# Performance work log

Measured on AMD Instinct MI355X. Metric: run time of the kernel, lower is better.

## Reference

```python
import jax, jax.numpy as jnp
import numpy as np

B, N, F = 8, 512, 128
H, U = 4, 32
LEAKY_ALPHA = 0.2

def setup_inputs() -> dict:
    key = jax.random.key(0)
    k1, k2, k3, k4 = jax.random.split(key, 4)
    inputs = jax.random.normal(k1, (B, N, F), dtype=jnp.float32)
    # glorot-ish scaled params
    W_src = jax.random.normal(k2, (H, F, U), dtype=jnp.float32) * (2.0 / (F + U)) ** 0.5
    W_dst = jax.random.normal(k3, (H, F, U), dtype=jnp.float32) * (2.0 / (F + U)) ** 0.5
    a = jax.random.normal(k4, (H, U, 1), dtype=jnp.float32) * (2.0 / (U + 1)) ** 0.5
    return {"inputs": inputs, "W_src": W_src, "W_dst": W_dst, "a": a}

def reference(inputs, W_src, W_dst, a):
    # GATv2, eval mode (no dropout). Loop over the small fixed head count to
    # keep peak memory at one (B,N,N,U) pairwise tensor at a time, matching
    # the original per-head loop.
    outs = []
    for h in range(W_src.shape[0]):
        h_src = inputs @ W_src[h]          # (B, N, U)
        h_dst = inputs @ W_dst[h]          # (B, N, U)
        # pairwise[b,i,j,:] = h_src[b,i] + h_dst[b,j]
        pair = jax.nn.leaky_relu(h_src[:, :, None, :] + h_dst[:, None, :, :],
                                 negative_slope=LEAKY_ALPHA)  # (B,N,N,U)
        scores = jnp.einsum('biju,u->bij', pair, a[h, :, 0])   # (B,N,N)
        attn = jax.nn.softmax(scores, axis=-1)
        outs.append(attn @ h_src)          # (B,N,U) -- weighted sum of h_src
    return jnp.concatenate(outs, axis=-1)  # concat_heads=True -> (B,N,H*U)
```

## Files before the change

### kernel.cpp

```cpp
#include <hip/hip_runtime.h>
#include <hip/hip_bf16.h>

#define B_ 8
#define N_ 512
#define F_ 128
#define H_ 4
#define U_ 32
#define LEAKY_ALPHA 0.2f
#define PS 520

typedef __attribute__((ext_vector_type(8))) short short8;
typedef __attribute__((ext_vector_type(4))) float f32x4;

static __device__ __forceinline__ short f2bf_s(float x) {
    __hip_bfloat16 hv = __float2bfloat16(x);
    return *reinterpret_cast<short*>(&hv);
}
static __device__ __forceinline__ float bf2f_s(short v) {
    return __uint_as_float(((unsigned)(unsigned short)v) << 16);
}

__global__ __launch_bounds__(256) void proj_kernel(
    const float* __restrict__ x, const float* __restrict__ Wsrc,
    const float* __restrict__ Wdst, const float* __restrict__ a,
    float* __restrict__ hsrc, float* __restrict__ hdstNT,
    float* __restrict__ Drow, float* __restrict__ ascaled,
    short* __restrict__ hsrcT)
{
    __shared__ float4 xlds[8 * 32];
    const int t  = threadIdx.x;
    const int r0 = blockIdx.x * 8;

    const float4* xg = (const float4*)x + (size_t)r0 * 32;
    xlds[t] = xg[t];
    __syncthreads();

    const int u     = t & 31;
    const int h     = (t >> 5) & 3;
    const int which = t >> 7;
    const float* W  = (which ? Wdst : Wsrc) + h * (F_ * U_) + u;

    float acc[8];
#pragma unroll
    for (int r = 0; r < 8; ++r) acc[r] = 0.f;

#pragma unroll 2
    for (int fc = 0; fc < 32; ++fc) {
        const float w0 = W[(4 * fc + 0) * U_];
        const float w1 = W[(4 * fc + 1) * U_];
        const float w2 = W[(4 * fc + 2) * U_];
        const float w3 = W[(4 * fc + 3) * U_];
#pragma unroll
        for (int r = 0; r < 8; ++r) {
            const float4 xv = xlds[r * 32 + fc];
            float s = acc[r];
            s = fmaf(xv.x, w0, s);
            s = fmaf(xv.y, w1, s);
            s = fmaf(xv.z, w2, s);
            s = fmaf(xv.w, w3, s);
            acc[r] = s;
        }
    }

    const float av = a[h * U_ + u];
    if (which == 1 && blockIdx.x == 0)
        ascaled[h * U_ + u] = (1.f - LEAKY_ALPHA) * av;

    const int b  = r0 >> 9;
    const int n0 = r0 & (N_ - 1);
    const int bh = b * H_ + h;

    if (which == 0) {
        short8 pk;
#pragma unroll
        for (int r = 0; r < 8; ++r) {
            const size_t base = ((size_t)(bh * N_ + n0 + r) << 5) + u;
            hsrc[base] = acc[r];
            pk[r] = f2bf_s(acc[r]);
        }
        *(short8*)&hsrcT[((size_t)(bh * U_) + u) * N_ + n0] = pk;
    } else {
        float4 v0, v1;
        v0.x = -acc[0]; v0.y = -acc[1]; v0.z = -acc[2]; v0.w = -acc[3];
        v1.x = -acc[4]; v1.y = -acc[5]; v1.z = -acc[6]; v1.w = -acc[7];
        float* dst = hdstNT + ((size_t)(bh * U_) + u) * N_ + n0;
        *(float4*)dst       = v0;
        *(float4*)(dst + 4) = v1;
#pragma unroll
        for (int r = 0; r < 8; ++r) {
            float v = acc[r] * av;
            v += __shfl_xor(v, 1);
            v += __shfl_xor(v, 2);
            v += __shfl_xor(v, 4);
            v += __shfl_xor(v, 8);
            v += __shfl_xor(v, 16);
            if (u == 0) Drow[bh * N_ + n0 + r] = v;
        }
    }
}

__global__ __launch_bounds__(512, 4) void attn_kernel(
    const float* __restrict__ hsrc, const float* __restrict__ hdstNT,
    const float* __restrict__ Drow, const float* __restrict__ ascaled,
    const short* __restrict__ hsrcT, float* __restrict__ out)
{
    __shared__ __align__(16) short pbf[16 * PS];
    __shared__ f32x4 scr[8][64];
    __shared__ float lfin[16];

    const int t    = threadIdx.x;
    const int L    = t & 63;
    const int w    = __builtin_amdgcn_readfirstlane(t >> 6);
    const int tile = blockIdx.x & 31;
    const int bh   = blockIdx.x >> 5;
    const int h    = bh & 3;
    const int b    = bh >> 2;
    const size_t bhN = (size_t)bh * N_;
    const int ig0  = tile * 16;
    const int j    = t;

    const float* dT = hdstNT + ((size_t)bh * U_) * N_ + j;
#define DL(k) float d##k = dT[(k) * N_];
    DL(0) DL(1) DL(2) DL(3) DL(4) DL(5) DL(6) DL(7)
    DL(8) DL(9) DL(10) DL(11) DL(12) DL(13) DL(14) DL(15)
    DL(16) DL(17) DL(18) DL(19) DL(20) DL(21) DL(22) DL(23)
    DL(24) DL(25) DL(26) DL(27) DL(28) DL(29) DL(30) DL(31)
#undef DL
#define PIN4(a0,a1,a2,a3) asm volatile("" : "+v"(a0), "+v"(a1), "+v"(a2), "+v"(a3));
    PIN4(d0,d1,d2,d3)     PIN4(d4,d5,d6,d7)
    PIN4(d8,d9,d10,d11)   PIN4(d12,d13,d14,d15)
    PIN4(d16,d17,d18,d19) PIN4(d20,d21,d22,d23)
    PIN4(d24,d25,d26,d27) PIN4(d28,d29,d30,d31)
#undef PIN4

    const float Dj = Drow[bhN + j];
    const float* sB = hsrc + ((bhN + ig0) << 5);
    const float* aS = ascaled + h * U_;

#define TERM(k, dk, accv) accv = fmaf(aS[k], fmaxf(sR[k], dk), accv);
#pragma unroll 2
    for (int i = 0; i < 16; ++i) {
        const float* sR = sB + (i << 5);
        float acA = 0.f, acB = 0.f;
        TERM(0,  d0,  acA) TERM(1,  d1,  acB) TERM(2,  d2,  acA) TERM(3,  d3,  acB)
        TERM(4,  d4,  acA) TERM(5,  d5,  acB) TERM(6,  d6,  acA) TERM(7,  d7,  acB)
        TERM(8,  d8,  acA) TERM(9,  d9,  acB) TERM(10, d10, acA) TERM(11, d11, acB)
        TERM(12, d12, acA) TERM(13, d13, acB) TERM(14, d14, acA) TERM(15, d15, acB)
        TERM(16, d16, acA) TERM(17, d17, acB) TERM(18, d18, acA) TERM(19, d19, acB)
        TERM(20, d20, acA) TERM(21, d21, acB) TERM(22, d22, acA) TERM(23, d23, acB)
        TERM(24, d24, acA) TERM(25, d25, acB) TERM(26, d26, acA) TERM(27, d27, acB)
        TERM(28, d28, acA) TERM(29, d29, acB) TERM(30, d30, acA) TERM(31, d31, acB)
        const float e = __expf(Dj + acA + acB);
        pbf[i * PS + j] = f2bf_s(e);
    }
#undef TERM
    __syncthreads();

    {
        const int ri = t >> 5;
        const int rg = t & 31;
        const short8* pr = (const short8*)(pbf + ri * PS + rg * 16);
        const short8 pa = pr[0];
        const short8 pb = pr[1];
        float sum = 0.f;
#pragma unroll
        for (int k = 0; k < 8; ++k) sum += bf2f_s(pa[k]) + bf2f_s(pb[k]);
        sum += __shfl_xor(sum, 1);
        sum += __shfl_xor(sum, 2);
        sum += __shfl_xor(sum, 4);
        sum += __shfl_xor(sum, 8);
        sum += __shfl_xor(sum, 16);
        if (rg == 0) lfin[ri] = __builtin_amdgcn_rcpf(sum);
    }

    const int m  = L & 15;
    const int kq = L >> 4;
    const int nt = w & 1;
    const int ks = w >> 1;
    const short* Ap = pbf + m * PS + ks * 128 + kq * 8;
    const short* Bp = hsrcT + ((size_t)bh * U_ + nt * 16 + m) * N_ + ks * 128 + kq * 8;

    f32x4 acc = {0.f, 0.f, 0.f, 0.f};
#pragma unroll
    for (int st = 0; st < 4; ++st) {
        const short8 af = *(const short8*)(Ap + st * 32);
        const short8 bf = *(const short8*)(Bp + st * 32);
        acc = __builtin_amdgcn_mfma_f32_16x16x32_bf16(af, bf, acc, 0, 0, 0);
    }
    scr[w][L] = acc;
    __syncthreads();

    if (w < 2) {
        f32x4 s0 = scr[w][L];
        const f32x4 s1 = scr[w + 2][L];
        const f32x4 s2 = scr[w + 4][L];
        const f32x4 s3 = scr[w + 6][L];
        s0 += s1; s0 += s2; s0 += s3;
#pragma unroll
        for (int r = 0; r < 4; ++r) {
            const int il = kq * 4 + r;
            out[((size_t)(b * N_ + ig0 + il)) * (H_ * U_) + h * U_ + w * 16 + m]
                = s0[r] * lfin[il];
        }
    }
}

extern "C" void kernel_launch(void* const* d_in, const int* in_sizes, int n_in,
                              void* d_out, int out_size, void* d_ws, size_t ws_size,
                              hipStream_t stream) {
    const float* x    = (const float*)d_in[0];
    const float* Wsrc = (const float*)d_in[1];
    const float* Wdst = (const float*)d_in[2];
    const float* a    = (const float*)d_in[3];

    float* ws      = (float*)d_ws;
    float* hsrc    = ws;
    float* hdstNT  = hsrc + (size_t)B_ * H_ * N_ * U_;
    float* Drow    = hdstNT + (size_t)B_ * H_ * U_ * N_;
    float* ascaled = Drow + (size_t)B_ * H_ * N_;
    short* hsrcT   = (short*)(ascaled + H_ * U_);

    proj_kernel<<<(B_ * N_) / 8, 256, 0, stream>>>(x, Wsrc, Wdst, a,
                                                   hsrc, hdstNT, Drow, ascaled,
                                                   hsrcT);
    attn_kernel<<<B_ * H_ * (N_ / 16), 512, 0, stream>>>(hsrc, hdstNT, Drow,
                                                         ascaled, hsrcT,
                                                         (float*)d_out);
}
```

Before: 98.72 us.

## Compute pairwise GATv2 scores in packed fp16 with fdot2 and exp2

Stores h_src and negated h_dst in fp16 instead of fp32, so the score loop can do packed fp16 max and v_dot2 accumulation into fp32, roughly halving the VALU instruction count in the dominant pairwise loop. The 1/ln2 factor is folded into the attention vector and the row term so a native exp2 replaces expf. Workspace traffic and register pressure also drop, since 16 packed registers replace 32. The cost is lower precision in the pre-activation values and the attention weights.

```diff
diff --git a/kernel.cpp b/kernel.cpp
--- a/kernel.cpp
+++ b/kernel.cpp
@@ -1,5 +1,6 @@
 #include <hip/hip_runtime.h>
 #include <hip/hip_bf16.h>
+#include <hip/hip_fp16.h>
 
 #define B_ 8
 #define N_ 512
@@ -8,9 +9,13 @@
 #define U_ 32
 #define LEAKY_ALPHA 0.2f
 #define PS 520
+#define RCPLN2 1.4426950408889634f
 
 typedef __attribute__((ext_vector_type(8))) short short8;
 typedef __attribute__((ext_vector_type(4))) float f32x4;
+typedef _Float16 h2 __attribute__((ext_vector_type(2)));
+typedef unsigned int u32;
+typedef unsigned short u16;
 
 static __device__ __forceinline__ short f2bf_s(float x) {
     __hip_bfloat16 hv = __float2bfloat16(x);
@@ -19,12 +24,19 @@
 static __device__ __forceinline__ float bf2f_s(short v) {
     return __uint_as_float(((unsigned)(unsigned short)v) << 16);
 }
+static __device__ __forceinline__ u16 f2h_s(float x) {
+    __half h = __float2half(x);
+    return *reinterpret_cast<u16*>(&h);
+}
+static __device__ __forceinline__ h2 u2h2(u32 v) {
+    return __builtin_bit_cast(h2, v);
+}
 
 __global__ __launch_bounds__(256) void proj_kernel(
     const float* __restrict__ x, const float* __restrict__ Wsrc,
     const float* __restrict__ Wdst, const float* __restrict__ a,
-    float* __restrict__ hsrc, float* __restrict__ hdstNT,
-    float* __restrict__ Drow, float* __restrict__ ascaled,
+    float* __restrict__ Drow, u16* __restrict__ a2h,
+    u16* __restrict__ sf16, u16* __restrict__ dT16,
     short* __restrict__ hsrcT)
 {
     __shared__ float4 xlds[8 * 32];
@@ -64,7 +76,7 @@
 
     const float av = a[h * U_ + u];
     if (which == 1 && blockIdx.x == 0)
-        ascaled[h * U_ + u] = (1.f - LEAKY_ALPHA) * av;
+        a2h[h * U_ + u] = f2h_s((1.f - LEAKY_ALPHA) * av * RCPLN2);
 
     const int b  = r0 >> 9;
     const int n0 = r0 & (N_ - 1);
@@ -73,19 +85,16 @@
     if (which == 0) {
         short8 pk;
 #pragma unroll
-        for (int r = 0; r < 8; ++r) {
-            const size_t base = ((size_t)(bh * N_ + n0 + r) << 5) + u;
-            hsrc[base] = acc[r];
-            pk[r] = f2bf_s(acc[r]);
-        }
+        for (int r = 0; r < 8; ++r) pk[r] = f2bf_s(acc[r]);
         *(short8*)&hsrcT[((size_t)(bh * U_) + u) * N_ + n0] = pk;
+#pragma unroll
+        for (int r = 0; r < 8; ++r)
+            sf16[((size_t)(bh * N_ + n0 + r) << 5) + u] = f2h_s(acc[r]);
     } else {
-        float4 v0, v1;
-        v0.x = -acc[0]; v0.y = -acc[1]; v0.z = -acc[2]; v0.w = -acc[3];
-        v1.x = -acc[4]; v1.y = -acc[5]; v1.z = -acc[6]; v1.w = -acc[7];
-        float* dst = hdstNT + ((size_t)(bh * U_) + u) * N_ + n0;
-        *(float4*)dst       = v0;
-        *(float4*)(dst + 4) = v1;
+        short8 dk;
+#pragma unroll
+        for (int r = 0; r < 8; ++r) dk[r] = (short)f2h_s(-acc[r]);
+        *(short8*)&dT16[((size_t)(bh * U_) + u) * N_ + n0] = dk;
 #pragma unroll
         for (int r = 0; r < 8; ++r) {
             float v = acc[r] * av;
@@ -94,14 +103,14 @@
             v += __shfl_xor(v, 4);
             v += __shfl_xor(v, 8);
             v += __shfl_xor(v, 16);
-            if (u == 0) Drow[bh * N_ + n0 + r] = v;
+            if (u == 0) Drow[bh * N_ + n0 + r] = v * RCPLN2;
         }
     }
 }
 
 __global__ __launch_bounds__(512, 4) void attn_kernel(
-    const float* __restrict__ hsrc, const float* __restrict__ hdstNT,
-    const float* __restrict__ Drow, const float* __restrict__ ascaled,
+    const float* __restrict__ Drow, const u16* __restrict__ a2h,
+    const u32* __restrict__ sf16, const u16* __restrict__ dT16,
     const short* __restrict__ hsrcT, float* __restrict__ out)
 {
     __shared__ __align__(16) short pbf[16 * PS];
@@ -119,41 +128,43 @@
     const int ig0  = tile * 16;
     const int j    = t;
 
-    const float* dT = hdstNT + ((size_t)bh * U_) * N_ + j;
-#define DL(k) float d##k = dT[(k) * N_];
-    DL(0) DL(1) DL(2) DL(3) DL(4) DL(5) DL(6) DL(7)
-    DL(8) DL(9) DL(10) DL(11) DL(12) DL(13) DL(14) DL(15)
-    DL(16) DL(17) DL(18) DL(19) DL(20) DL(21) DL(22) DL(23)
-    DL(24) DL(25) DL(26) DL(27) DL(28) DL(29) DL(30) DL(31)
-#undef DL
+    const u16* dT = dT16 + ((size_t)bh * U_) * N_ + j;
+#define DL2(p) u32 dd##p = (u32)dT[(2*(p)) * N_] | ((u32)dT[(2*(p)+1) * N_] << 16);
+    DL2(0) DL2(1) DL2(2)  DL2(3)  DL2(4)  DL2(5)  DL2(6)  DL2(7)
+    DL2(8) DL2(9) DL2(10) DL2(11) DL2(12) DL2(13) DL2(14) DL2(15)
+#undef DL2
 #define PIN4(a0,a1,a2,a3) asm volatile("" : "+v"(a0), "+v"(a1), "+v"(a2), "+v"(a3));
-    PIN4(d0,d1,d2,d3)     PIN4(d4,d5,d6,d7)
-    PIN4(d8,d9,d10,d11)   PIN4(d12,d13,d14,d15)
-    PIN4(d16,d17,d18,d19) PIN4(d20,d21,d22,d23)
-    PIN4(d24,d25,d26,d27) PIN4(d28,d29,d30,d31)
+    PIN4(dd0,dd1,dd2,dd3)     PIN4(dd4,dd5,dd6,dd7)
+    PIN4(dd8,dd9,dd10,dd11)   PIN4(dd12,dd13,dd14,dd15)
 #undef PIN4
 
     const float Dj = Drow[bhN + j];
-    const float* sB = hsrc + ((bhN + ig0) << 5);
-    const float* aS = ascaled + h * U_;
-
-#define TERM(k, dk, accv) accv = fmaf(aS[k], fmaxf(sR[k], dk), accv);
+    const u32* sB = sf16 + ((bhN + (size_t)ig0) << 4);
+    const h2* aH = (const h2*)a2h + h * (U_ / 2);
+    const h2 a0 = aH[0],  a1 = aH[1],  a2 = aH[2],  a3 = aH[3];
+    const h2 a4 = aH[4],  a5 = aH[5],  a6 = aH[6],  a7 = aH[7];
+    const h2 a8 = aH[8],  a9 = aH[9],  a10 = aH[10], a11 = aH[11];
+    const h2 a12 = aH[12], a13 = aH[13], a14 = aH[14], a15 = aH[15];
+
+#define PK(k, ak, ddk, accv) {                                                \
+    const h2 m_ = __builtin_elementwise_max(sR[k], u2h2(ddk));                \
+    accv = __builtin_amdgcn_fdot2(ak, m_, accv, false); }
 #pragma unroll 2
     for (int i = 0; i < 16; ++i) {
-        const float* sR = sB + (i << 5);
-        float acA = 0.f, acB = 0.f;
-        TERM(0,  d0,  acA) TERM(1,  d1,  acB) TERM(2,  d2,  acA) TERM(3,  d3,  acB)
-        TERM(4,  d4,  acA) TERM(5,  d5,  acB) TERM(6,  d6,  acA) TERM(7,  d7,  acB)
-        TERM(8,  d8,  acA) TERM(9,  d9,  acB) TERM(10, d10, acA) TERM(11, d11, acB)
-        TERM(12, d12, acA) TERM(13, d13, acB) TERM(14, d14, acA) TERM(15, d15, acB)
-        TERM(16, d16, acA) TERM(17, d17, acB) TERM(18, d18, acA) TERM(19, d19, acB)
-        TERM(20, d20, acA) TERM(21, d21, acB) TERM(22, d22, acA) TERM(23, d23, acB)
-        TERM(24, d24, acA) TERM(25, d25, acB) TERM(26, d26, acA) TERM(27, d27, acB)
-        TERM(28, d28, acA) TERM(29, d29, acB) TERM(30, d30, acA) TERM(31, d31, acB)
-        const float e = __expf(Dj + acA + acB);
+        const h2* sR = (const h2*)(sB + (i << 4));
+        float acA = Dj, acB = 0.f;
+        PK(0,  a0,  dd0,  acA) PK(1,  a1,  dd1,  acB)
+        PK(2,  a2,  dd2,  acA) PK(3,  a3,  dd3,  acB)
+        PK(4,  a4,  dd4,  acA) PK(5,  a5,  dd5,  acB)
+        PK(6,  a6,  dd6,  acA) PK(7,  a7,  dd7,  acB)
+        PK(8,  a8,  dd8,  acA) PK(9,  a9,  dd9,  acB)
+        PK(10, a10, dd10, acA) PK(11, a11, dd11, acB)
+        PK(12, a12, dd12, acA) PK(13, a13, dd13, acB)
+        PK(14, a14, dd14, acA) PK(15, a15, dd15, acB)
+        const float e = __builtin_amdgcn_exp2f(acA + acB);
         pbf[i * PS + j] = f2bf_s(e);
     }
-#undef TERM
+#undef PK
     __syncthreads();
 
     {
@@ -213,17 +224,18 @@
     const float* Wdst = (const float*)d_in[2];
     const float* a    = (const float*)d_in[3];
 
-    float* ws      = (float*)d_ws;
-    float* hsrc    = ws;
-    float* hdstNT  = hsrc + (size_t)B_ * H_ * N_ * U_;
-    float* Drow    = hdstNT + (size_t)B_ * H_ * U_ * N_;
-    float* ascaled = Drow + (size_t)B_ * H_ * N_;
-    short* hsrcT   = (short*)(ascaled + H_ * U_);
+    float* ws    = (float*)d_ws;
+    float* Drow  = ws;
+    u16*   a2h   = (u16*)(Drow + (size_t)B_ * H_ * N_);
+    u16*   sf16  = a2h + 128;
+    u16*   dT16  = sf16 + (size_t)B_ * H_ * N_ * U_;
+    short* hsrcT = (short*)(dT16 + (size_t)B_ * H_ * U_ * N_);
 
     proj_kernel<<<(B_ * N_) / 8, 256, 0, stream>>>(x, Wsrc, Wdst, a,
-                                                   hsrc, hdstNT, Drow, ascaled,
+                                                   Drow, a2h, sf16, dT16,
                                                    hsrcT);
-    attn_kernel<<<B_ * H_ * (N_ / 16), 512, 0, stream>>>(hsrc, hdstNT, Drow,
-                                                         ascaled, hsrcT,
+    attn_kernel<<<B_ * H_ * (N_ / 16), 512, 0, stream>>>(Drow, a2h,
+                                                         (const u32*)sf16,
+                                                         dT16, hsrcT,
                                                          (float*)d_out);
 }
```

Measured after the change: 88.86 us. 10.0% less time.
